# Kernel optimization log

Hardware: AMD Instinct MI355X
Metric: run time of the kernel (lower is better)

Reference implementation:

```python
import jax, jax.numpy as jnp
import numpy as np

MAX_VALUE = 127.0  # 2**(8-1)-1, signed int8 symmetric quantization


def _quantize_int8(t, amax):
    # TensorQuantizer (fake_quant=False): scale = max_value/amax, round, clamp to int8 range.
    s = MAX_VALUE / amax
    return jnp.clip(jnp.round(t * s), -MAX_VALUE, MAX_VALUE)  # integer-valued float32


def setup_inputs() -> dict:
    key = jax.random.key(0)
    kx, kw, kb = jax.random.split(key, 3)
    x = jax.random.normal(kx, (32, 32, 224, 224), dtype=jnp.float32)
    weight = jax.random.normal(kw, (64, 32, 3, 3), dtype=jnp.float32) * 0.06  # kaiming-ish scale
    fan_in = 32 * 3 * 3
    bound = 1.0 / np.sqrt(fan_in)
    bias = jax.random.uniform(kb, (64,), dtype=jnp.float32, minval=-bound, maxval=bound)
    return {"x": x, "weight": weight, "bias": bias}


def reference(x, weight, bias):
    # Calibrated per-tensor amax (histogram calibrator approximated by abs-max)
    amax_x = jax.lax.stop_gradient(jnp.max(jnp.abs(x)))
    amax_w = jax.lax.stop_gradient(jnp.max(jnp.abs(weight)))

    qx = _quantize_int8(x, amax_x)       # int8 values held in fp32
    qw = _quantize_int8(weight, amax_w)

    # Exact int32 systolic conv: accumulation magnitude <= 127*127*288 < 2**24,
    # so fp32 conv reproduces the int32 accumulate bit-exactly.
    out_i32 = jax.lax.conv_general_dilated(
        qx, qw,
        window_strides=(1, 1),
        padding=((1, 1), (1, 1)),
        dimension_numbers=("NCHW", "OIHW", "NCHW"),
        feature_group_count=1,
    )  # [N, Cout, H, W]

    scale = (MAX_VALUE / amax_x) * (MAX_VALUE / amax_w)
    out = out_i32 / scale
    return out + bias[None, :, None, None]
```

## Files before the change

kernel.cpp:

```cpp
#include <hip/hip_runtime.h>
#include <stdint.h>

typedef int v4i __attribute__((ext_vector_type(4)));
typedef float v4f __attribute__((ext_vector_type(4)));

#define BN 32
#define CI 32
#define CO 64
#define HH 224
#define WW 224

#define AMAX_BLOCKS 2048

static const size_t QW_BYTES  = 3 * 64 * 128;
static const size_t AMAX_OFF  = QW_BYTES;
static const size_t PART_OFF  = AMAX_OFF + 128;

__device__ __forceinline__ int swz(int o) { return o ^ ((o >> 3) & 0x70); }

__global__ __launch_bounds__(256) void k_amax_x(const float4* __restrict__ x4,
                                                float* __restrict__ partials, long n4) {
    float m = 0.f;
    long i = (long)blockIdx.x * blockDim.x + threadIdx.x;
    long stride = (long)gridDim.x * blockDim.x;
    for (; i < n4; i += stride) {
        float4 v = x4[i];
        m = fmaxf(m, fmaxf(fmaxf(fabsf(v.x), fabsf(v.y)), fmaxf(fabsf(v.z), fabsf(v.w))));
    }
    for (int o = 32; o > 0; o >>= 1) m = fmaxf(m, __shfl_xor(m, o));
    __shared__ float sm[4];
    if ((threadIdx.x & 63) == 0) sm[threadIdx.x >> 6] = m;
    __syncthreads();
    if (threadIdx.x == 0)
        partials[blockIdx.x] = fmaxf(fmaxf(sm[0], sm[1]), fmaxf(sm[2], sm[3]));
}

__global__ __launch_bounds__(256) void k_quant_w(const float* __restrict__ w,
                                                 const float* __restrict__ partials,
                                                 signed char* __restrict__ qw,
                                                 float* __restrict__ amax_pair) {
    __shared__ __align__(16) signed char qs[24576];
    __shared__ float smx[4], smw[4];
    __shared__ float s_ax, s_aw;
    int t = threadIdx.x;
    for (int i = t; i < 1536; i += 256) ((v4i*)qs)[i] = (v4i){0, 0, 0, 0};

    float mx = 0.f;
    for (int i = t; i < AMAX_BLOCKS; i += 256) mx = fmaxf(mx, partials[i]);
    float mw = 0.f;
    const float4* w4 = (const float4*)w;
    for (int i = t; i < 4608; i += 256) {
        float4 v = w4[i];
        mw = fmaxf(mw, fmaxf(fmaxf(fabsf(v.x), fabsf(v.y)), fmaxf(fabsf(v.z), fabsf(v.w))));
    }
    for (int o = 32; o > 0; o >>= 1) {
        mx = fmaxf(mx, __shfl_xor(mx, o));
        mw = fmaxf(mw, __shfl_xor(mw, o));
    }
    if ((t & 63) == 0) { smx[t >> 6] = mx; smw[t >> 6] = mw; }
    __syncthreads();
    if (t == 0) {
        s_ax = fmaxf(fmaxf(smx[0], smx[1]), fmaxf(smx[2], smx[3]));
        s_aw = fmaxf(fmaxf(smw[0], smw[1]), fmaxf(smw[2], smw[3]));
        amax_pair[0] = s_ax;
        amax_pair[1] = s_aw;
    }
    __syncthreads();
    float s = 127.0f / s_aw;
    for (int i4 = t; i4 < 4608; i4 += 256) {
        float4 v = w4[i4];
        float e[4] = {v.x, v.y, v.z, v.w};
#pragma unroll
        for (int j = 0; j < 4; j++) {
            int idx = i4 * 4 + j;
            int kw = idx % 3;
            int kh = (idx / 3) % 3;
            int ci = (idx / 9) % 32;
            int o  = idx / 288;
            float q = rintf(e[j] * s);
            q = fminf(127.f, fmaxf(-127.f, q));
            qs[kh * 8192 + o * 128 + kw * 32 + ci] = (signed char)q;
        }
    }
    __syncthreads();
    for (int i = t; i < 1536; i += 256) ((v4i*)qw)[i] = ((const v4i*)qs)[i];
}

__device__ __forceinline__ void qpack_write(const float4 (&v)[4], bool valid, int gh,
                                            int cw, int cbase, float s_x,
                                            signed char* __restrict__ ldsb) {
    int pk[4] = {0, 0, 0, 0};
    if (valid) {
#pragma unroll
        for (int l = 0; l < 4; l++) {
            int q0 = (int)rintf(fminf(127.f, fmaxf(-127.f, v[l].x * s_x)));
            int q1 = (int)rintf(fminf(127.f, fmaxf(-127.f, v[l].y * s_x)));
            int q2 = (int)rintf(fminf(127.f, fmaxf(-127.f, v[l].z * s_x)));
            int q3 = (int)rintf(fminf(127.f, fmaxf(-127.f, v[l].w * s_x)));
            pk[0] |= (q0 & 255) << (8 * l);
            pk[1] |= (q1 & 255) << (8 * l);
            pk[2] |= (q2 & 255) << (8 * l);
            pk[3] |= (q3 & 255) << (8 * l);
        }
    }
#pragma unroll
    for (int j = 0; j < 4; j++)
        *(int*)&ldsb[swz((((gh & 3) * 120) + cw * 4 + j) * 32 + cbase)] = pk[j];
}

__global__ __launch_bounds__(256) void k_conv(const float* __restrict__ x,
                                              const signed char* __restrict__ qw,
                                              const float* __restrict__ bias,
                                              const float* __restrict__ amax_pair,
                                              float* __restrict__ out) {
    __shared__ __align__(16) signed char lds[4 * 120 * 32 + 4 * 16 * 116 * 4];
    float* ep = (float*)(lds + 15360);

    int b = blockIdx.x;
    int wt = b & 1;
    int hs = (b >> 1) & 7;
    int n = b >> 4;
    int w0 = wt * 112;
    int hstart = hs * 28;
    int t = threadIdx.x;
    int lane = t & 63;
    int wv = t >> 6;
    int r = lane & 15;
    int chunk = lane >> 4;
    int cout = wv * 16 + r;

    float ax = amax_pair[0];
    float aw = amax_pair[1];
    float s_x = 127.0f / ax;
    float scale = (127.0f / ax) * (127.0f / aw);
    float invs = 1.0f / scale;
    float bv = bias[cout];

    v4i bf[3][2];
#pragma unroll
    for (int dh = 0; dh < 3; dh++)
#pragma unroll
        for (int s = 0; s < 2; s++)
            bf[dh][s] = *(const v4i*)&qw[dh * 8192 + cout * 128 + s * 64 + chunk * 16];

#pragma unroll
    for (int k = 0; k < 4; k++) {
        int task = t + k * 256;
        if (task < 960) {
            int quad = task & 7;
            int rc = task >> 3;
            int cw = rc % 30;
            int row = rc / 30;
            int gh = hstart - 1 + row;
            int gw0 = w0 - 4 + cw * 4;
            int cbase = quad * 4;
            bool valid = ((unsigned)gh < 224u) && ((unsigned)gw0 < 224u);
            float4 v[4];
            if (valid) {
#pragma unroll
                for (int l = 0; l < 4; l++)
                    v[l] = *(const float4*)&x[((size_t)(n * CI + cbase + l) * HH + gh) * WW + gw0];
            }
            qpack_write(v, valid, gh, cw, cbase, s_x, lds);
        }
    }
    __syncthreads();

    float* epw = ep + wv * (16 * 116);

#pragma unroll 1
    for (int i = 0; i < 14; i++) {
        int h0 = hstart + 2 * i;
        bool pf = (i < 13);

        float4 ldA[4], ldB[4];
        int ghA = 0, cwA = 0, cbA = 0, ghB = 0, cwB = 0, cbB = 0;
        bool vA = false, vB = false, hasB = (t < 224);
        if (pf) {
            {
                int task = t;
                int quad = task & 7;
                int rc = task >> 3;
                cwA = rc % 30;
                int row = rc / 30;
                ghA = h0 + 3 + row;
                int gw0 = w0 - 4 + cwA * 4;
                cbA = quad * 4;
                vA = ((unsigned)ghA < 224u) && ((unsigned)gw0 < 224u);
                if (vA) {
#pragma unroll
                    for (int l = 0; l < 4; l++)
                        ldA[l] = *(const float4*)&x[((size_t)(n * CI + cbA + l) * HH + ghA) * WW + gw0];
                }
            }
            if (hasB) {
                int task = t + 256;
                int quad = task & 7;
                int rc = task >> 3;
                cwB = rc % 30;
                int row = rc / 30;
                ghB = h0 + 3 + row;
                int gw0 = w0 - 4 + cwB * 4;
                cbB = quad * 4;
                vB = ((unsigned)ghB < 224u) && ((unsigned)gw0 < 224u);
                if (vB) {
#pragma unroll
                    for (int l = 0; l < 4; l++)
                        ldB[l] = *(const float4*)&x[((size_t)(n * CI + cbB + l) * HH + ghB) * WW + gw0];
                }
            }
        }

        v4i acc[14];
#pragma unroll
        for (int m = 0; m < 14; m++) acc[m] = (v4i){0, 0, 0, 0};
#pragma unroll
        for (int dh = 0; dh < 3; dh++) {
#pragma unroll
            for (int s = 0; s < 2; s++) {
                int k16 = s * 64 + chunk * 16;
                int dw = k16 >> 5;
                if (dw > 2) dw = 2;
                int cih = (k16 >> 4) & 1;
#pragma unroll
                for (int m = 0; m < 14; m++) {
                    int gh = h0 - 1 + (m / 7) + dh;
                    int wl = 3 + (m % 7) * 16 + r + dw;
                    v4i af = *(const v4i*)&lds[swz((((gh & 3) * 120) + wl) * 32 + cih * 16)];
                    acc[m] = __builtin_amdgcn_mfma_i32_16x16x64_i8(af, bf[dh][s], acc[m], 0, 0, 0);
                }
            }
        }

#pragma unroll
        for (int half = 0; half < 2; half++) {
#pragma unroll
            for (int mm = 0; mm < 7; mm++) {
                int m = half * 7 + mm;
                float4 o;
                o.x = fmaf((float)acc[m][0], invs, bv);
                o.y = fmaf((float)acc[m][1], invs, bv);
                o.z = fmaf((float)acc[m][2], invs, bv);
                o.w = fmaf((float)acc[m][3], invs, bv);
                *(float4*)&epw[r * 116 + mm * 16 + chunk * 4] = o;
            }
            int hh = h0 + half;
#pragma unroll
            for (int it = 0; it < 7; it++) {
                int idx = it * 64 + lane;
                int co = idx / 28;
                int w4 = (idx % 28) * 4;
                v4f v = *(const v4f*)&epw[co * 116 + w4];
                __builtin_nontemporal_store(v,
                    (v4f*)&out[(((size_t)n * CO + wv * 16 + co) * HH + hh) * WW + w0 + w4]);
            }
        }

        __syncthreads();

        if (pf) {
            qpack_write(ldA, vA, ghA, cwA, cbA, s_x, lds);
            if (hasB) qpack_write(ldB, vB, ghB, cwB, cbB, s_x, lds);
        }
        __syncthreads();
    }
}

extern "C" void kernel_launch(void* const* d_in, const int* in_sizes, int n_in,
                              void* d_out, int out_size, void* d_ws, size_t ws_size,
                              hipStream_t stream) {
    const float* x = (const float*)d_in[0];
    const float* w = (const float*)d_in[1];
    const float* bias = (const float*)d_in[2];
    float* out = (float*)d_out;

    signed char* qw = (signed char*)d_ws;
    float* amax_pair = (float*)((char*)d_ws + AMAX_OFF);
    float* partials = (float*)((char*)d_ws + PART_OFF);

    long n4 = (long)BN * CI * HH * WW / 4;
    k_amax_x<<<AMAX_BLOCKS, 256, 0, stream>>>((const float4*)x, partials, n4);
    k_quant_w<<<1, 256, 0, stream>>>(w, partials, qw, amax_pair);
    k_conv<<<512, 256, 0, stream>>>(x, qw, bias, amax_pair, out);
}
```

Measured before the change: 151.9 us.

## Fuse weight quantization and amax reduction into conv kernel prologue

Removes the single-block weight-quantization kernel and has every conv block reduce the x-amax partials and the weight amax itself, then quantize and pack its own weight fragments directly from the fp32 weights. This drops a serial one-block launch and its kernel boundary between the amax pass and the conv. In exchange each of the 512 conv blocks redundantly reads 2048 partials and all 18K weights, and does per-lane scattered scalar weight loads in its prologue.

```diff
diff --git a/kernel.cpp b/kernel.cpp
--- a/kernel.cpp
+++ b/kernel.cpp
@@ -11,10 +11,6 @@
 #define WW 224
 
 #define AMAX_BLOCKS 2048
-
-static const size_t QW_BYTES  = 3 * 64 * 128;
-static const size_t AMAX_OFF  = QW_BYTES;
-static const size_t PART_OFF  = AMAX_OFF + 128;
 
 __device__ __forceinline__ int swz(int o) { return o ^ ((o >> 3) & 0x70); }
 
@@ -33,57 +29,6 @@
     __syncthreads();
     if (threadIdx.x == 0)
         partials[blockIdx.x] = fmaxf(fmaxf(sm[0], sm[1]), fmaxf(sm[2], sm[3]));
-}
-
-__global__ __launch_bounds__(256) void k_quant_w(const float* __restrict__ w,
-                                                 const float* __restrict__ partials,
-                                                 signed char* __restrict__ qw,
-                                                 float* __restrict__ amax_pair) {
-    __shared__ __align__(16) signed char qs[24576];
-    __shared__ float smx[4], smw[4];
-    __shared__ float s_ax, s_aw;
-    int t = threadIdx.x;
-    for (int i = t; i < 1536; i += 256) ((v4i*)qs)[i] = (v4i){0, 0, 0, 0};
-
-    float mx = 0.f;
-    for (int i = t; i < AMAX_BLOCKS; i += 256) mx = fmaxf(mx, partials[i]);
-    float mw = 0.f;
-    const float4* w4 = (const float4*)w;
-    for (int i = t; i < 4608; i += 256) {
-        float4 v = w4[i];
-        mw = fmaxf(mw, fmaxf(fmaxf(fabsf(v.x), fabsf(v.y)), fmaxf(fabsf(v.z), fabsf(v.w))));
-    }
-    for (int o = 32; o > 0; o >>= 1) {
-        mx = fmaxf(mx, __shfl_xor(mx, o));
-        mw = fmaxf(mw, __shfl_xor(mw, o));
-    }
-    if ((t & 63) == 0) { smx[t >> 6] = mx; smw[t >> 6] = mw; }
-    __syncthreads();
-    if (t == 0) {
-        s_ax = fmaxf(fmaxf(smx[0], smx[1]), fmaxf(smx[2], smx[3]));
-        s_aw = fmaxf(fmaxf(smw[0], smw[1]), fmaxf(smw[2], smw[3]));
-        amax_pair[0] = s_ax;
-        amax_pair[1] = s_aw;
-    }
-    __syncthreads();
-    float s = 127.0f / s_aw;
-    for (int i4 = t; i4 < 4608; i4 += 256) {
-        float4 v = w4[i4];
-        float e[4] = {v.x, v.y, v.z, v.w};
-#pragma unroll
-        for (int j = 0; j < 4; j++) {
-            int idx = i4 * 4 + j;
-            int kw = idx % 3;
-            int kh = (idx / 3) % 3;
-            int ci = (idx / 9) % 32;
-            int o  = idx / 288;
-            float q = rintf(e[j] * s);
-            q = fminf(127.f, fmaxf(-127.f, q));
-            qs[kh * 8192 + o * 128 + kw * 32 + ci] = (signed char)q;
-        }
-    }
-    __syncthreads();
-    for (int i = t; i < 1536; i += 256) ((v4i*)qw)[i] = ((const v4i*)qs)[i];
 }
 
 __device__ __forceinline__ void qpack_write(const float4 (&v)[4], bool valid, int gh,
@@ -109,12 +54,14 @@
 }
 
 __global__ __launch_bounds__(256) void k_conv(const float* __restrict__ x,
-                                              const signed char* __restrict__ qw,
+                                              const float* __restrict__ w,
                                               const float* __restrict__ bias,
-                                              const float* __restrict__ amax_pair,
+                                              const float* __restrict__ partials,
                                               float* __restrict__ out) {
     __shared__ __align__(16) signed char lds[4 * 120 * 32 + 4 * 16 * 116 * 4];
     float* ep = (float*)(lds + 15360);
+    __shared__ float smx[4], smw[4];
+    __shared__ float sax, saw;
 
     int b = blockIdx.x;
     int wt = b & 1;
@@ -129,19 +76,54 @@
     int chunk = lane >> 4;
     int cout = wv * 16 + r;
 
-    float ax = amax_pair[0];
-    float aw = amax_pair[1];
+    float mx = 0.f;
+    for (int i = t; i < AMAX_BLOCKS; i += 256) mx = fmaxf(mx, partials[i]);
+    float mw = 0.f;
+    const float4* w4 = (const float4*)w;
+    for (int i = t; i < 4608; i += 256) {
+        float4 v = w4[i];
+        mw = fmaxf(mw, fmaxf(fmaxf(fabsf(v.x), fabsf(v.y)), fmaxf(fabsf(v.z), fabsf(v.w))));
+    }
+    for (int o = 32; o > 0; o >>= 1) {
+        mx = fmaxf(mx, __shfl_xor(mx, o));
+        mw = fmaxf(mw, __shfl_xor(mw, o));
+    }
+    if ((t & 63) == 0) { smx[t >> 6] = mx; smw[t >> 6] = mw; }
+    __syncthreads();
+    if (t == 0) {
+        sax = fmaxf(fmaxf(smx[0], smx[1]), fmaxf(smx[2], smx[3]));
+        saw = fmaxf(fmaxf(smw[0], smw[1]), fmaxf(smw[2], smw[3]));
+    }
+    __syncthreads();
+    float ax = sax;
+    float aw = saw;
     float s_x = 127.0f / ax;
-    float scale = (127.0f / ax) * (127.0f / aw);
-    float invs = 1.0f / scale;
+    float s_w = 127.0f / aw;
+    float invs = 1.0f / ((127.0f / ax) * (127.0f / aw));
     float bv = bias[cout];
 
     v4i bf[3][2];
 #pragma unroll
-    for (int dh = 0; dh < 3; dh++)
-#pragma unroll
-        for (int s = 0; s < 2; s++)
-            bf[dh][s] = *(const v4i*)&qw[dh * 8192 + cout * 128 + s * 64 + chunk * 16];
+    for (int dh = 0; dh < 3; dh++) {
+#pragma unroll
+        for (int s = 0; s < 2; s++) {
+            int pk[4] = {0, 0, 0, 0};
+            int k16 = s * 64 + chunk * 16;
+            if (k16 < 96) {
+#pragma unroll
+                for (int j = 0; j < 16; j++) {
+                    int k = k16 + j;
+                    int ci = k & 31;
+                    int kw = k >> 5;
+                    float wval = w[((cout * 32 + ci) * 3 + dh) * 3 + kw];
+                    float q = rintf(wval * s_w);
+                    q = fminf(127.f, fmaxf(-127.f, q));
+                    pk[j >> 2] |= ((int)q & 255) << (8 * (j & 3));
+                }
+            }
+            bf[dh][s] = (v4i){pk[0], pk[1], pk[2], pk[3]};
+        }
+    }
 
 #pragma unroll
     for (int k = 0; k < 4; k++) {
@@ -249,10 +231,10 @@
             for (int it = 0; it < 7; it++) {
                 int idx = it * 64 + lane;
                 int co = idx / 28;
-                int w4 = (idx % 28) * 4;
-                v4f v = *(const v4f*)&epw[co * 116 + w4];
+                int w4i_ = (idx % 28) * 4;
+                v4f v = *(const v4f*)&epw[co * 116 + w4i_];
                 __builtin_nontemporal_store(v,
-                    (v4f*)&out[(((size_t)n * CO + wv * 16 + co) * HH + hh) * WW + w0 + w4]);
+                    (v4f*)&out[(((size_t)n * CO + wv * 16 + co) * HH + hh) * WW + w0 + w4i_]);
             }
         }
 
@@ -274,12 +256,9 @@
     const float* bias = (const float*)d_in[2];
     float* out = (float*)d_out;
 
-    signed char* qw = (signed char*)d_ws;
-    float* amax_pair = (float*)((char*)d_ws + AMAX_OFF);
-    float* partials = (float*)((char*)d_ws + PART_OFF);
+    float* partials = (float*)d_ws;
 
     long n4 = (long)BN * CI * HH * WW / 4;
     k_amax_x<<<AMAX_BLOCKS, 256, 0, stream>>>((const float4*)x, partials, n4);
-    k_quant_w<<<1, 256, 0, stream>>>(w, partials, qw, amax_pair);
-    k_conv<<<512, 256, 0, stream>>>(x, qw, bias, amax_pair, out);
-}
+    k_conv<<<512, 256, 0, stream>>>(x, w, bias, partials, out);
+}
```

Result: slower. 161.5 us (+6.4%).
